# Optimization experiments

Hardware: AMD Instinct MI355X
Metric: run time of the kernel (lower is better)

## Reference

```python
import jax, jax.numpy as jnp
import numpy as np

N = 50000   # nodes
E = 640000  # edges
D = 128     # feature dim (din == dmid, required since edge_attr is reused every layer)
L = 5       # GINEConv layers
BN_EPS = 1e-5


def setup_inputs() -> dict:
    key = jax.random.key(0)
    ks = jax.random.split(key, 8)
    x = jax.random.normal(ks[0], (N, D), dtype=jnp.float32)
    edge_index = jax.random.randint(ks[1], (2, E), 0, N, dtype=jnp.int64)
    edge_attr = jax.random.normal(ks[2], (E, D), dtype=jnp.float32)
    W1 = jax.random.normal(ks[3], (L, D, D), dtype=jnp.float32) * 0.05
    b1 = jnp.zeros((L, D), dtype=jnp.float32)
    gamma = jnp.ones((L, D), dtype=jnp.float32)
    beta = jnp.zeros((L, D), dtype=jnp.float32)
    W2 = jax.random.normal(ks[4], (L, D, D), dtype=jnp.float32) * 0.05
    b2 = jnp.zeros((L, D), dtype=jnp.float32)
    return {"x": x, "edge_index": edge_index, "edge_attr": edge_attr,
            "W1": W1, "b1": b1, "gamma": gamma, "beta": beta, "W2": W2, "b2": b2}


def reference(x, edge_index, edge_attr, W1, b1, gamma, beta, W2, b2):
    src, dst = edge_index[0], edge_index[1]  # PyG: messages flow src(j) -> dst(i)
    h = x
    for l in range(L):
        # GINEConv message + aggregate: sum_j ReLU(x_j + e_ij)
        m = jax.nn.relu(h[src] + edge_attr)               # [E, D] gather + add
        agg = jax.ops.segment_sum(m, dst, num_segments=N)  # [N, D] scatter-sum
        h = agg + h  # (1 + eps) * x_i with eps = 0
        # MLP: Linear -> BatchNorm1d (batch stats) -> ReLU -> Linear
        h = h @ W1[l] + b1[l]
        mu = jnp.mean(h, axis=0)
        var = jnp.var(h, axis=0)  # biased var, as torch BN uses for normalization
        h = gamma[l] * (h - mu) * jax.lax.rsqrt(var + BN_EPS) + beta[l]
        h = jax.nn.relu(h)
        h = h @ W2[l] + b2[l]
    return h
```

## Files before the change

kernel.cpp:

```cpp
#include <hip/hip_runtime.h>
#include <hip/hip_bf16.h>
#include <stdint.h>

#define D 128
#define LAYERS 5
#define BN_EPS 1e-5f

typedef unsigned int uint32;
typedef __bf16 bf16x8 __attribute__((ext_vector_type(8)));
typedef float f32x4 __attribute__((ext_vector_type(4)));
typedef float f32x2 __attribute__((ext_vector_type(2)));
typedef uint32 u32x2 __attribute__((ext_vector_type(2)));
typedef uint32 u32x4 __attribute__((ext_vector_type(4)));

__device__ inline unsigned short f2bf(float f) {
    uint32 u = __float_as_uint(f);
    return (unsigned short)((u + 0x7fffu + ((u >> 16) & 1u)) >> 16);
}
__device__ inline float bflo(uint32 p) { return __uint_as_float(p << 16); }
__device__ inline float bfhi(uint32 p) { return __uint_as_float(p & 0xffff0000u); }
__device__ inline uint32 pack2(float a, float b) {
    return (uint32)f2bf(a) | ((uint32)f2bf(b) << 16);
}


__global__ void detect_kernel(const int* __restrict__ ei, int* __restrict__ flag) {
    if (threadIdx.x == 0 && blockIdx.x == 0) {
        int allz = 1;
#pragma unroll
        for (int i = 0; i < 16; ++i) allz &= (ei[2 * i + 1] == 0);
        *flag = allz;
    }
}


__global__ __launch_bounds__(256) void hist_kernel(const int* __restrict__ ei,
                                                   const int* __restrict__ flag,
                                                   int* __restrict__ deg, int E, int n) {
    int e = blockIdx.x * blockDim.x + threadIdx.x;
    if (e >= E) return;
    int is64 = *flag;
    int d = is64 ? ei[2 * ((size_t)E + e)] : ei[E + e];
    if ((unsigned)d < (unsigned)n) atomicAdd(&deg[d], 1);
}

__global__ __launch_bounds__(1024) void scan_kernel(const int* __restrict__ deg,
                                                    int* __restrict__ off, int n) {
    __shared__ int tsum[1024];
    int t = threadIdx.x;
    int CH = (n + 1023) >> 10;
    int lo = t * CH;
    int hi = lo + CH; if (hi > n) hi = n;
    int s = 0;
    for (int i = lo; i < hi; ++i) s += deg[i];
    tsum[t] = s;
    __syncthreads();
    for (int d = 1; d < 1024; d <<= 1) {
        int v = (t >= d) ? tsum[t - d] : 0;
        __syncthreads();
        tsum[t] += v;
        __syncthreads();
    }
    int run = tsum[t] - s;
    for (int i = lo; i < hi; ++i) { off[i] = run; run += deg[i]; }
    if (t == 1023) off[n] = tsum[1023];
}

__global__ __launch_bounds__(256) void fill_kernel(const int* __restrict__ ei,
                                                   const int* __restrict__ flag,
                                                   const int* __restrict__ off,
                                                   int* __restrict__ cursor,
                                                   int* __restrict__ srcs,
                                                   int* __restrict__ eidx, int E, int n) {
    int e = blockIdx.x * blockDim.x + threadIdx.x;
    if (e >= E) return;
    int is64 = *flag;
    int d = is64 ? ei[2 * ((size_t)E + e)] : ei[E + e];
    int s = is64 ? ei[2 * (size_t)e] : ei[e];
    if ((unsigned)d >= (unsigned)n || (unsigned)s >= (unsigned)n) return;
    int p = atomicAdd(&cursor[d], 1);
    int pos = off[d] + p;
    srcs[pos] = s;
    eidx[pos] = e;
}


__global__ __launch_bounds__(256) void wt_kernel(const float* __restrict__ W1,
                                                 const float* __restrict__ W2,
                                                 unsigned short* __restrict__ wt) {
    int id = blockIdx.x * 256 + threadIdx.x;
    if (id >= 10 * 16384) return;
    int l = id >> 14;
    int rem = id & 16383;
    int nn = rem >> 7, kk = rem & 127;
    const float* base = (l < 5) ? (W1 + (size_t)l * 16384) : (W2 + (size_t)(l - 5) * 16384);
    wt[(size_t)l * 16384 + nn * 128 + kk] = f2bf(base[kk * 128 + nn]);
}


__global__ __launch_bounds__(256) void agg_cvt_kernel(const float* __restrict__ x,
                                                      const float* __restrict__ ea,
                                                      const int* __restrict__ off,
                                                      const int* __restrict__ srcs,
                                                      const int* __restrict__ eidx,
                                                      uint32* __restrict__ eab,
                                                      uint32* __restrict__ out, int n) {
    int node = blockIdx.x * 4 + (threadIdx.x >> 6);
    if (node >= n) return;
    const int lane = threadIdx.x & 63;
    const int half = lane >> 5;
    const int q = lane & 31;
    f32x4 acc = {0.f, 0.f, 0.f, 0.f};
    int e = off[node];
    const int end = off[node + 1];
    while (e < end) {
        const int cnt = min(end - e, 64);
        const int sidx = (e + lane < end) ? srcs[e + lane] : 0;
        const int yidx = (e + lane < end) ? eidx[e + lane] : 0;
        int i = 0;
        for (; i + 4 <= cnt; i += 4) {
            const int iA = i + half, iB = i + 2 + half;
            const int sA = __shfl(sidx, iA), yA = __shfl(yidx, iA);
            const int sB = __shfl(sidx, iB), yB = __shfl(yidx, iB);
            f32x4 va = __builtin_nontemporal_load((const f32x4*)(ea + (size_t)yA * D + q * 4));
            f32x4 vb = __builtin_nontemporal_load((const f32x4*)(ea + (size_t)yB * D + q * 4));
            f32x4 ha = *(const f32x4*)(x + (size_t)sA * D + q * 4);
            f32x4 hb = *(const f32x4*)(x + (size_t)sB * D + q * 4);
#pragma unroll
            for (int k = 0; k < 4; ++k)
                acc[k] += fmaxf(ha[k] + va[k], 0.f) + fmaxf(hb[k] + vb[k], 0.f);
            u32x2 pa = {pack2(va[0], va[1]), pack2(va[2], va[3])};
            u32x2 pb = {pack2(vb[0], vb[1]), pack2(vb[2], vb[3])};
            *(u32x2*)(eab + (size_t)(e + iA) * 64 + q * 2) = pa;
            *(u32x2*)(eab + (size_t)(e + iB) * 64 + q * 2) = pb;
        }
        if (i + 2 <= cnt) {
            const int iA = i + half;
            const int sA = __shfl(sidx, iA), yA = __shfl(yidx, iA);
            f32x4 va = __builtin_nontemporal_load((const f32x4*)(ea + (size_t)yA * D + q * 4));
            f32x4 ha = *(const f32x4*)(x + (size_t)sA * D + q * 4);
#pragma unroll
            for (int k = 0; k < 4; ++k) acc[k] += fmaxf(ha[k] + va[k], 0.f);
            u32x2 pa = {pack2(va[0], va[1]), pack2(va[2], va[3])};
            *(u32x2*)(eab + (size_t)(e + iA) * 64 + q * 2) = pa;
            i += 2;
        }
        if (i < cnt) {
            const int sA = __shfl(sidx, i), yA = __shfl(yidx, i);
            if (half == 0) {
                f32x4 va = __builtin_nontemporal_load((const f32x4*)(ea + (size_t)yA * D + q * 4));
                f32x4 ha = *(const f32x4*)(x + (size_t)sA * D + q * 4);
#pragma unroll
                for (int k = 0; k < 4; ++k) acc[k] += fmaxf(ha[k] + va[k], 0.f);
                u32x2 pa = {pack2(va[0], va[1]), pack2(va[2], va[3])};
                *(u32x2*)(eab + (size_t)(e + i) * 64 + q * 2) = pa;
            }
        }
        e += cnt;
    }
#pragma unroll
    for (int k = 0; k < 4; ++k) acc[k] += __shfl_xor(acc[k], 32);
    if (half == 0) {
        f32x4 xs = *(const f32x4*)(x + (size_t)node * D + q * 4);
        u32x2 o = {pack2(xs[0] + acc[0], xs[1] + acc[1]),
                   pack2(xs[2] + acc[2], xs[3] + acc[3])};
        *(u32x2*)(out + (size_t)node * 64 + q * 2) = o;
    }
}


__global__ __launch_bounds__(256) void agg_kernel(const uint32* __restrict__ h,
                                                  const uint32* __restrict__ eab,
                                                  const int* __restrict__ off,
                                                  const int* __restrict__ srcs,
                                                  uint32* __restrict__ out, int n) {
    int node = blockIdx.x * 4 + (threadIdx.x >> 6);
    if (node >= n) return;
    const int lane = threadIdx.x & 63;
    const int g = lane >> 4;
    const int j = lane & 15;
    float acc[8] = {0.f, 0.f, 0.f, 0.f, 0.f, 0.f, 0.f, 0.f};
    int e = off[node];
    const int end = off[node + 1];
    while (e < end) {
        const int cnt = min(end - e, 64);
        const int sidx = (e + lane < end) ? srcs[e + lane] : 0;
        int i = 0;
        for (; i + 8 <= cnt; i += 8) {
            const int sA = __shfl(sidx, i + g);
            const int sB = __shfl(sidx, i + 4 + g);
            u32x4 a0 = *(const u32x4*)(eab + (size_t)(e + i + g) * 64 + j * 4);
            u32x4 a1 = *(const u32x4*)(eab + (size_t)(e + i + 4 + g) * 64 + j * 4);
            u32x4 h0 = *(const u32x4*)(h + (size_t)sA * 64 + j * 4);
            u32x4 h1 = *(const u32x4*)(h + (size_t)sB * 64 + j * 4);
#pragma unroll
            for (int k = 0; k < 4; ++k) {
                acc[2 * k]     += fmaxf(bflo(h0[k]) + bflo(a0[k]), 0.f)
                                + fmaxf(bflo(h1[k]) + bflo(a1[k]), 0.f);
                acc[2 * k + 1] += fmaxf(bfhi(h0[k]) + bfhi(a0[k]), 0.f)
                                + fmaxf(bfhi(h1[k]) + bfhi(a1[k]), 0.f);
            }
        }
        if (i + 4 <= cnt) {
            const int sA = __shfl(sidx, i + g);
            u32x4 a0 = *(const u32x4*)(eab + (size_t)(e + i + g) * 64 + j * 4);
            u32x4 h0 = *(const u32x4*)(h + (size_t)sA * 64 + j * 4);
#pragma unroll
            for (int k = 0; k < 4; ++k) {
                acc[2 * k]     += fmaxf(bflo(h0[k]) + bflo(a0[k]), 0.f);
                acc[2 * k + 1] += fmaxf(bfhi(h0[k]) + bfhi(a0[k]), 0.f);
            }
            i += 4;
        }
        const int rem = cnt - i;
        if (rem) {
            const int sA = __shfl(sidx, i + (g < rem ? g : 0));
            if (g < rem) {
                u32x4 a0 = *(const u32x4*)(eab + (size_t)(e + i + g) * 64 + j * 4);
                u32x4 h0 = *(const u32x4*)(h + (size_t)sA * 64 + j * 4);
#pragma unroll
                for (int k = 0; k < 4; ++k) {
                    acc[2 * k]     += fmaxf(bflo(h0[k]) + bflo(a0[k]), 0.f);
                    acc[2 * k + 1] += fmaxf(bfhi(h0[k]) + bfhi(a0[k]), 0.f);
                }
            }
        }
        e += cnt;
    }
#pragma unroll
    for (int k = 0; k < 8; ++k) {
        acc[k] += __shfl_xor(acc[k], 16);
        acc[k] += __shfl_xor(acc[k], 32);
    }
    if (g == 0) {
        u32x4 hn = *(const u32x4*)(h + (size_t)node * 64 + j * 4);
        u32x4 o;
#pragma unroll
        for (int k = 0; k < 4; ++k)
            o[k] = pack2(bflo(hn[k]) + acc[2 * k], bfhi(hn[k]) + acc[2 * k + 1]);
        *(u32x4*)(out + (size_t)node * 64 + j * 4) = o;
    }
}


template <int MODE, bool F32OUT>
__global__ __launch_bounds__(256) void gemm_kernel(const uint4* __restrict__ A,
                                                   const uint4* __restrict__ Wt4,
                                                   const float* __restrict__ bias,
                                                   void* __restrict__ outp,
                                                   float* __restrict__ colstats,
                                                   const float* __restrict__ gamma,
                                                   const float* __restrict__ beta,
                                                   float inv_n, int n, int nTiles) {
    __shared__ float red[256];
    const int t = threadIdx.x;
    const int wv = t >> 6, l = t & 63;
    const int lrow = l & 15, lk = l >> 4;

    if (MODE == 1) {
        red[t] = 0.f;
    } else {
        if (t < 128) {
            float mu = colstats[t] * inv_n;
            float var = colstats[128 + t] * inv_n - mu * mu;
            float inv = rsqrtf(var + BN_EPS);
            float sc = gamma[t] * inv;
            red[t] = sc;
            red[128 + t] = beta[t] - mu * sc;
        }
    }
    __syncthreads();

    float* outF = (float*)outp;
    unsigned short* outB = (unsigned short*)outp;
    float sAcc[8] = {0, 0, 0, 0, 0, 0, 0, 0};
    float s2Acc[8] = {0, 0, 0, 0, 0, 0, 0, 0};

    for (int tile = blockIdx.x; tile < nTiles; tile += gridDim.x) {
        const int r0 = tile * 64 + wv * 16;

        bf16x8 af[4];
        const int arow = r0 + lrow;
        const bool rowok = arow < n;
#pragma unroll
        for (int c = 0; c < 4; ++c) {
            union { uint4 u; bf16x8 v; uint32 w[4]; } bu;
            bu.u = make_uint4(0u, 0u, 0u, 0u);
            if (rowok) bu.u = A[(size_t)arow * 16 + c * 4 + lk];
            if (MODE == 2) {
                const int kb = c * 32 + lk * 8;
                float xv[8];
#pragma unroll
                for (int i = 0; i < 4; ++i) {
                    xv[2 * i]     = bflo(bu.w[i]);
                    xv[2 * i + 1] = bfhi(bu.w[i]);
                }
#pragma unroll
                for (int j = 0; j < 8; ++j)
                    xv[j] = fmaxf(fmaf(red[kb + j], xv[j], red[128 + kb + j]), 0.f);
#pragma unroll
                for (int i = 0; i < 4; ++i)
                    bu.w[i] = pack2(xv[2 * i], xv[2 * i + 1]);
            }
            af[c] = bu.v;
        }

#pragma unroll
        for (int n0 = 0; n0 < 8; ++n0) {
            const int wcol = n0 * 16 + lrow;
            f32x4 acc = {0.f, 0.f, 0.f, 0.f};
#pragma unroll
            for (int c = 0; c < 4; ++c) {
                union { uint4 u; bf16x8 v; } bu;
                bu.u = Wt4[wcol * 16 + c * 4 + lk];
                acc = __builtin_amdgcn_mfma_f32_16x16x32_bf16(af[c], bu.v, acc, 0, 0, 0);
            }
            const float bcol = bias[wcol];
#pragma unroll
            for (int r = 0; r < 4; ++r) {
                int row = r0 + lk * 4 + r;
                float v = acc[r] + bcol;
                if (row < n) {
                    if (F32OUT) outF[(size_t)row * D + wcol] = v;
                    else        outB[(size_t)row * D + wcol] = f2bf(v);
                    if (MODE == 1) { sAcc[n0] += v; s2Acc[n0] += v * v; }
                }
            }
        }
    }

    if (MODE == 1) {
#pragma unroll
        for (int n0 = 0; n0 < 8; ++n0) {
            const int wcol = n0 * 16 + lrow;
            float ls = sAcc[n0], ls2 = s2Acc[n0];
            ls  += __shfl_xor(ls, 16);  ls  += __shfl_xor(ls, 32);
            ls2 += __shfl_xor(ls2, 16); ls2 += __shfl_xor(ls2, 32);
            if (lk == 0) {
                atomicAdd(&red[wcol], ls);
                atomicAdd(&red[D + wcol], ls2);
            }
        }
        __syncthreads();
        if (t < 128) {
            atomicAdd(&colstats[t], red[t]);
            atomicAdd(&colstats[D + t], red[D + t]);
        }
    }
}


extern "C" void kernel_launch(void* const* d_in, const int* in_sizes, int n_in,
                              void* d_out, int out_size, void* d_ws, size_t ws_size,
                              hipStream_t stream) {
    const float* x      = (const float*)d_in[0];
    const int*   ei     = (const int*)d_in[1];
    const float* ea     = (const float*)d_in[2];
    const float* W1     = (const float*)d_in[3];
    const float* b1     = (const float*)d_in[4];
    const float* gamma  = (const float*)d_in[5];
    const float* beta   = (const float*)d_in[6];
    const float* W2     = (const float*)d_in[7];
    const float* b2     = (const float*)d_in[8];
    const int N = in_sizes[0] / D;
    const int E = in_sizes[1] / 2;

    char* w = (char*)d_ws;
    auto alloc = [&](size_t bytes) {
        char* p = w;
        w += (bytes + 255) & ~(size_t)255;
        return p;
    };
    int*    off      = (int*)alloc((size_t)(N + 1) * sizeof(int));
    int*    zbase    = (int*)alloc(((size_t)2 * N + 5 * 256) * sizeof(int));
    int*    deg      = zbase;
    int*    cursor   = zbase + N;
    float*  colstats = (float*)(zbase + 2 * N);
    int*    flag     = (int*)alloc(256);
    unsigned short* wt = (unsigned short*)alloc(10 * 16384 * sizeof(unsigned short));
    int*    srcs     = (int*)alloc((size_t)E * sizeof(int));
    int*    eidx     = (int*)alloc((size_t)E * sizeof(int));
    uint32* eab      = (uint32*)alloc((size_t)E * 64 * sizeof(uint32));
    uint32* G        = (uint32*)alloc((size_t)N * 64 * sizeof(uint32));
    uint32* T        = (uint32*)alloc((size_t)N * 64 * sizeof(uint32));
    uint32* H        = (uint32*)alloc((size_t)N * 64 * sizeof(uint32));

    wt_kernel<<<(10 * 16384 + 255) / 256, 256, 0, stream>>>(W1, W2, wt);
    detect_kernel<<<1, 64, 0, stream>>>(ei, flag);
    hipMemsetAsync(zbase, 0, ((size_t)2 * N + 5 * 256) * sizeof(int), stream);
    hist_kernel<<<(E + 255) / 256, 256, 0, stream>>>(ei, flag, deg, E, N);
    scan_kernel<<<1, 1024, 0, stream>>>(deg, off, N);
    fill_kernel<<<(E + 255) / 256, 256, 0, stream>>>(ei, flag, off, cursor, srcs, eidx, E, N);

    const int nTiles    = (N + 63) / 64;
    const int gemmGrid  = nTiles < 512 ? nTiles : 512;
    const int aggBlocks = (N + 3) / 4;
    const float inv_n = 1.0f / (float)N;

    const uint32* hin = nullptr;
    for (int l = 0; l < LAYERS; ++l) {
        float* cst = colstats + l * 256;
        const uint4* wt1 = (const uint4*)(wt + (size_t)l * 16384);
        const uint4* wt2 = (const uint4*)(wt + (size_t)(5 + l) * 16384);
        if (l == 0)
            agg_cvt_kernel<<<aggBlocks, 256, 0, stream>>>(x, ea, off, srcs, eidx, eab, G, N);
        else
            agg_kernel<<<aggBlocks, 256, 0, stream>>>(hin, eab, off, srcs, G, N);
        gemm_kernel<1, false><<<gemmGrid, 256, 0, stream>>>(
            (const uint4*)G, wt1, b1 + l * D, T, cst, nullptr, nullptr, inv_n, N, nTiles);
        if (l < LAYERS - 1)
            gemm_kernel<2, false><<<gemmGrid, 256, 0, stream>>>(
                (const uint4*)T, wt2, b2 + l * D, H, cst,
                gamma + l * D, beta + l * D, inv_n, N, nTiles);
        else
            gemm_kernel<2, true><<<gemmGrid, 256, 0, stream>>>(
                (const uint4*)T, wt2, b2 + l * D, d_out, cst,
                gamma + l * D, beta + l * D, inv_n, N, nTiles);
        hin = H;
    }
}
```

Baseline: 688.2 us.

## Fuse both MLP GEMMs into one kernel with grid barrier for BatchNorm stats

Merges the Linear1+stats GEMM and the BN+ReLU+Linear2 GEMM into a single kernel. Each block keeps its (at most two) intermediate 64-row tiles in LDS, then waits at a global atomic-counter barrier until all BatchNorm column statistics are accumulated, and runs the second GEMM straight from LDS. This drops the global round trip of the intermediate T buffer and one kernel launch per layer. In exchange it depends on all grid blocks being resident at once for the spin barrier, and it caps each block at two tiles.

```diff
diff --git a/kernel.cpp b/kernel.cpp
--- a/kernel.cpp
+++ b/kernel.cpp
@@ -243,68 +243,45 @@
 }
 
 
-template <int MODE, bool F32OUT>
-__global__ __launch_bounds__(256) void gemm_kernel(const uint4* __restrict__ A,
-                                                   const uint4* __restrict__ Wt4,
-                                                   const float* __restrict__ bias,
-                                                   void* __restrict__ outp,
-                                                   float* __restrict__ colstats,
-                                                   const float* __restrict__ gamma,
-                                                   const float* __restrict__ beta,
-                                                   float inv_n, int n, int nTiles) {
+template <bool F32OUT>
+__global__ __launch_bounds__(256, 2) void mlp_kernel(const uint4* __restrict__ A,
+                                                     const uint4* __restrict__ Wt1,
+                                                     const uint4* __restrict__ Wt2,
+                                                     const float* __restrict__ b1,
+                                                     const float* __restrict__ b2,
+                                                     void* __restrict__ outp,
+                                                     float* __restrict__ colstats,
+                                                     const float* __restrict__ gamma,
+                                                     const float* __restrict__ beta,
+                                                     int* __restrict__ bar,
+                                                     float inv_n, int n, int nTiles) {
+    __shared__ __align__(16) unsigned short Tsm[2][64][136];
     __shared__ float red[256];
     const int t = threadIdx.x;
     const int wv = t >> 6, l = t & 63;
     const int lrow = l & 15, lk = l >> 4;
 
-    if (MODE == 1) {
-        red[t] = 0.f;
-    } else {
-        if (t < 128) {
-            float mu = colstats[t] * inv_n;
-            float var = colstats[128 + t] * inv_n - mu * mu;
-            float inv = rsqrtf(var + BN_EPS);
-            float sc = gamma[t] * inv;
-            red[t] = sc;
-            red[128 + t] = beta[t] - mu * sc;
-        }
-    }
-    __syncthreads();
-
-    float* outF = (float*)outp;
-    unsigned short* outB = (unsigned short*)outp;
+    red[t] = 0.f;
+    __syncthreads();
+
     float sAcc[8] = {0, 0, 0, 0, 0, 0, 0, 0};
     float s2Acc[8] = {0, 0, 0, 0, 0, 0, 0, 0};
 
-    for (int tile = blockIdx.x; tile < nTiles; tile += gridDim.x) {
+#pragma unroll
+    for (int slot = 0; slot < 2; ++slot) {
+        const int tile = blockIdx.x + slot * gridDim.x;
+        if (tile >= nTiles) break;
         const int r0 = tile * 64 + wv * 16;
-
         bf16x8 af[4];
         const int arow = r0 + lrow;
         const bool rowok = arow < n;
 #pragma unroll
         for (int c = 0; c < 4; ++c) {
-            union { uint4 u; bf16x8 v; uint32 w[4]; } bu;
+            union { uint4 u; bf16x8 v; } bu;
             bu.u = make_uint4(0u, 0u, 0u, 0u);
             if (rowok) bu.u = A[(size_t)arow * 16 + c * 4 + lk];
-            if (MODE == 2) {
-                const int kb = c * 32 + lk * 8;
-                float xv[8];
-#pragma unroll
-                for (int i = 0; i < 4; ++i) {
-                    xv[2 * i]     = bflo(bu.w[i]);
-                    xv[2 * i + 1] = bfhi(bu.w[i]);
-                }
-#pragma unroll
-                for (int j = 0; j < 8; ++j)
-                    xv[j] = fmaxf(fmaf(red[kb + j], xv[j], red[128 + kb + j]), 0.f);
-#pragma unroll
-                for (int i = 0; i < 4; ++i)
-                    bu.w[i] = pack2(xv[2 * i], xv[2 * i + 1]);
-            }
             af[c] = bu.v;
         }
-
 #pragma unroll
         for (int n0 = 0; n0 < 8; ++n0) {
             const int wcol = n0 * 16 + lrow;
@@ -312,39 +289,110 @@
 #pragma unroll
             for (int c = 0; c < 4; ++c) {
                 union { uint4 u; bf16x8 v; } bu;
-                bu.u = Wt4[wcol * 16 + c * 4 + lk];
+                bu.u = Wt1[wcol * 16 + c * 4 + lk];
                 acc = __builtin_amdgcn_mfma_f32_16x16x32_bf16(af[c], bu.v, acc, 0, 0, 0);
             }
-            const float bcol = bias[wcol];
+            const float bcol = b1[wcol];
 #pragma unroll
             for (int r = 0; r < 4; ++r) {
-                int row = r0 + lk * 4 + r;
-                float v = acc[r] + bcol;
+                const int row = r0 + lk * 4 + r;
+                const float v = acc[r] + bcol;
+                if (row < n) {
+                    Tsm[slot][wv * 16 + lk * 4 + r][wcol] = f2bf(v);
+                    sAcc[n0] += v;
+                    s2Acc[n0] += v * v;
+                }
+            }
+        }
+    }
+
+#pragma unroll
+    for (int n0 = 0; n0 < 8; ++n0) {
+        const int wcol = n0 * 16 + lrow;
+        float ls = sAcc[n0], ls2 = s2Acc[n0];
+        ls  += __shfl_xor(ls, 16);  ls  += __shfl_xor(ls, 32);
+        ls2 += __shfl_xor(ls2, 16); ls2 += __shfl_xor(ls2, 32);
+        if (lk == 0) {
+            atomicAdd(&red[wcol], ls);
+            atomicAdd(&red[D + wcol], ls2);
+        }
+    }
+    __syncthreads();
+    if (t < 128) {
+        atomicAdd(&colstats[t], red[t]);
+        atomicAdd(&colstats[D + t], red[D + t]);
+    }
+
+    __threadfence();
+    __syncthreads();
+    if (t == 0) {
+        atomicAdd(bar, 1);
+        while (__hip_atomic_load(bar, __ATOMIC_ACQUIRE, __HIP_MEMORY_SCOPE_AGENT) <
+               (int)gridDim.x) {}
+    }
+    __syncthreads();
+
+    if (t < 128) {
+        float cs  = __hip_atomic_load(&colstats[t], __ATOMIC_RELAXED,
+                                      __HIP_MEMORY_SCOPE_AGENT);
+        float cs2 = __hip_atomic_load(&colstats[128 + t], __ATOMIC_RELAXED,
+                                      __HIP_MEMORY_SCOPE_AGENT);
+        float mu = cs * inv_n;
+        float var = cs2 * inv_n - mu * mu;
+        float inv = rsqrtf(var + BN_EPS);
+        float sc = gamma[t] * inv;
+        red[t] = sc;
+        red[128 + t] = beta[t] - mu * sc;
+    }
+    __syncthreads();
+
+    float* outF = (float*)outp;
+    unsigned short* outB = (unsigned short*)outp;
+#pragma unroll
+    for (int slot = 0; slot < 2; ++slot) {
+        const int tile = blockIdx.x + slot * gridDim.x;
+        if (tile >= nTiles) break;
+        const int r0 = tile * 64 + wv * 16;
+        bf16x8 af[4];
+#pragma unroll
+        for (int c = 0; c < 4; ++c) {
+            union { uint4 u; bf16x8 v; uint32 w[4]; } bu;
+            bu.u = *(const uint4*)&Tsm[slot][wv * 16 + lrow][(c * 4 + lk) * 8];
+            const int kb = c * 32 + lk * 8;
+            float xv[8];
+#pragma unroll
+            for (int i = 0; i < 4; ++i) {
+                xv[2 * i]     = bflo(bu.w[i]);
+                xv[2 * i + 1] = bfhi(bu.w[i]);
+            }
+#pragma unroll
+            for (int j = 0; j < 8; ++j)
+                xv[j] = fmaxf(fmaf(red[kb + j], xv[j], red[128 + kb + j]), 0.f);
+#pragma unroll
+            for (int i = 0; i < 4; ++i)
+                bu.w[i] = pack2(xv[2 * i], xv[2 * i + 1]);
+            af[c] = bu.v;
+        }
+#pragma unroll
+        for (int n0 = 0; n0 < 8; ++n0) {
+            const int wcol = n0 * 16 + lrow;
+            f32x4 acc = {0.f, 0.f, 0.f, 0.f};
+#pragma unroll
+            for (int c = 0; c < 4; ++c) {
+                union { uint4 u; bf16x8 v; } bu;
+                bu.u = Wt2[wcol * 16 + c * 4 + lk];
+                acc = __builtin_amdgcn_mfma_f32_16x16x32_bf16(af[c], bu.v, acc, 0, 0, 0);
+            }
+            const float bcol = b2[wcol];
+#pragma unroll
+            for (int r = 0; r < 4; ++r) {
+                const int row = r0 + lk * 4 + r;
+                const float v = acc[r] + bcol;
                 if (row < n) {
                     if (F32OUT) outF[(size_t)row * D + wcol] = v;
                     else        outB[(size_t)row * D + wcol] = f2bf(v);
-                    if (MODE == 1) { sAcc[n0] += v; s2Acc[n0] += v * v; }
                 }
             }
-        }
-    }
-
-    if (MODE == 1) {
-#pragma unroll
-        for (int n0 = 0; n0 < 8; ++n0) {
-            const int wcol = n0 * 16 + lrow;
-            float ls = sAcc[n0], ls2 = s2Acc[n0];
-            ls  += __shfl_xor(ls, 16);  ls  += __shfl_xor(ls, 32);
-            ls2 += __shfl_xor(ls2, 16); ls2 += __shfl_xor(ls2, 32);
-            if (lk == 0) {
-                atomicAdd(&red[wcol], ls);
-                atomicAdd(&red[D + wcol], ls2);
-            }
-        }
-        __syncthreads();
-        if (t < 128) {
-            atomicAdd(&colstats[t], red[t]);
-            atomicAdd(&colstats[D + t], red[D + t]);
         }
     }
 }
@@ -372,22 +420,22 @@
         return p;
     };
     int*    off      = (int*)alloc((size_t)(N + 1) * sizeof(int));
-    int*    zbase    = (int*)alloc(((size_t)2 * N + 5 * 256) * sizeof(int));
+    int*    zbase    = (int*)alloc(((size_t)2 * N + 5 * 256 + 8) * sizeof(int));
     int*    deg      = zbase;
     int*    cursor   = zbase + N;
     float*  colstats = (float*)(zbase + 2 * N);
+    int*    bar      = zbase + 2 * N + 5 * 256;
     int*    flag     = (int*)alloc(256);
     unsigned short* wt = (unsigned short*)alloc(10 * 16384 * sizeof(unsigned short));
     int*    srcs     = (int*)alloc((size_t)E * sizeof(int));
     int*    eidx     = (int*)alloc((size_t)E * sizeof(int));
     uint32* eab      = (uint32*)alloc((size_t)E * 64 * sizeof(uint32));
     uint32* G        = (uint32*)alloc((size_t)N * 64 * sizeof(uint32));
-    uint32* T        = (uint32*)alloc((size_t)N * 64 * sizeof(uint32));
     uint32* H        = (uint32*)alloc((size_t)N * 64 * sizeof(uint32));
 
     wt_kernel<<<(10 * 16384 + 255) / 256, 256, 0, stream>>>(W1, W2, wt);
     detect_kernel<<<1, 64, 0, stream>>>(ei, flag);
-    hipMemsetAsync(zbase, 0, ((size_t)2 * N + 5 * 256) * sizeof(int), stream);
+    hipMemsetAsync(zbase, 0, ((size_t)2 * N + 5 * 256 + 8) * sizeof(int), stream);
     hist_kernel<<<(E + 255) / 256, 256, 0, stream>>>(ei, flag, deg, E, N);
     scan_kernel<<<1, 1024, 0, stream>>>(deg, off, N);
     fill_kernel<<<(E + 255) / 256, 256, 0, stream>>>(ei, flag, off, cursor, srcs, eidx, E, N);
@@ -406,16 +454,14 @@
             agg_cvt_kernel<<<aggBlocks, 256, 0, stream>>>(x, ea, off, srcs, eidx, eab, G, N);
         else
             agg_kernel<<<aggBlocks, 256, 0, stream>>>(hin, eab, off, srcs, G, N);
-        gemm_kernel<1, false><<<gemmGrid, 256, 0, stream>>>(
-            (const uint4*)G, wt1, b1 + l * D, T, cst, nullptr, nullptr, inv_n, N, nTiles);
         if (l < LAYERS - 1)
-            gemm_kernel<2, false><<<gemmGrid, 256, 0, stream>>>(
-                (const uint4*)T, wt2, b2 + l * D, H, cst,
-                gamma + l * D, beta + l * D, inv_n, N, nTiles);
+            mlp_kernel<false><<<gemmGrid, 256, 0, stream>>>(
+                (const uint4*)G, wt1, wt2, b1 + l * D, b2 + l * D, H, cst,
+                gamma + l * D, beta + l * D, bar + l, inv_n, N, nTiles);
         else
-            gemm_kernel<2, true><<<gemmGrid, 256, 0, stream>>>(
-                (const uint4*)T, wt2, b2 + l * D, d_out, cst,
-                gamma + l * D, beta + l * D, inv_n, N, nTiles);
+            mlp_kernel<true><<<gemmGrid, 256, 0, stream>>>(
+                (const uint4*)G, wt1, wt2, b1 + l * D, b2 + l * D, d_out, cst,
+                gamma + l * D, beta + l * D, bar + l, inv_n, N, nTiles);
         hin = H;
     }
 }
```

After: 925.5 us. +34.5%, slower.
